# Performance work log

Measured on AMD Instinct MI355X. Metric: run time of the kernel, lower is better.

The kernel has to match this reference:

```python
import jax, jax.numpy as jnp
import numpy as np

P = 1024  # n_prototypes
D = 512   # embed_dim
B = 65536 # batch
EPS = 1e-12  # torch F.normalize eps


def _l2_normalize(x):
    # matches torch.nn.functional.normalize(x, dim=-1): x / max(||x||, eps)
    n = jnp.linalg.norm(x, axis=-1, keepdims=True)
    return x / jnp.maximum(n, EPS)


def setup_inputs() -> dict:
    key = jax.random.key(0)
    k1, k2 = jax.random.split(key)
    query_emb = jax.random.normal(k1, (B, D), dtype=jnp.float32)
    centroid_emb = jax.random.normal(k2, (P, D), dtype=jnp.float32)
    return {"query_emb": query_emb, "centroid_emb": centroid_emb}


def reference(query_emb, centroid_emb):
    q = _l2_normalize(query_emb)           # (B, D)
    c = _l2_normalize(centroid_emb)        # (P, D)
    logits = jnp.einsum('bd,pd->bp', q, c) # (B, P) cosine similarities
    hard_assignment = jnp.argmax(logits, axis=-1)              # (B,)
    hard_one_hot = jax.nn.one_hot(hard_assignment, P, dtype=logits.dtype)
    soft = jax.nn.softmax(logits, axis=-1)                     # (B, P)
    # straight-through: forward value = hard one-hot, gradient flows via soft
    routing_probs = hard_one_hot + soft - jax.lax.stop_gradient(soft)
    context_emb = jnp.einsum('bp,pd->bd', routing_probs, centroid_emb)  # (B, D)
    return context_emb, hard_assignment, routing_probs
```

## Files before the change

### kernel.cpp

```cpp
#include <hip/hip_runtime.h>
#include <hip/hip_bf16.h>
#include <climits>
#include <cstdint>

#define NB 65536
#define NP 1024
#define ND 512

#define MARGIN 4e-3f

typedef _Float16 f16x8 __attribute__((ext_vector_type(8)));
typedef float    f32x4 __attribute__((ext_vector_type(4)));

__device__ inline void load_lds16(const void* g, void* l) {
    __builtin_amdgcn_global_load_lds(
        (const __attribute__((address_space(1))) void*)g,
        (__attribute__((address_space(3))) void*)l, 16, 0, 0);
}

__global__ void centroid_rnorm_kernel(const float* __restrict__ cent,
                                      float* __restrict__ rnorm) {
    const int row  = blockIdx.x * 4 + (threadIdx.x >> 6);
    const int lane = threadIdx.x & 63;
    const float4* cr = (const float4*)(cent + (size_t)row * ND);
    float4 a = cr[2 * lane];
    float4 b = cr[2 * lane + 1];
    float s = a.x * a.x + a.y * a.y + a.z * a.z + a.w * a.w
            + b.x * b.x + b.y * b.y + b.z * b.z + b.w * b.w;
#pragma unroll
    for (int off = 32; off > 0; off >>= 1)
        s += __shfl_down(s, off, 64);
    if (lane == 0)
        rnorm[row] = 1.0f / fmaxf(sqrtf(s), 1e-12f);
}

__global__ void convertQ_kernel(const float* __restrict__ Q,
                                _Float16* __restrict__ Qp) {
    const size_t t = (size_t)blockIdx.x * 256 + threadIdx.x;
    const size_t base = t * 8;
    const float4* s = (const float4*)(Q + base);
    float4 x0 = s[0], x1 = s[1];
    float xs[8] = {x0.x, x0.y, x0.z, x0.w, x1.x, x1.y, x1.z, x1.w};
    f16x8 hi;
#pragma unroll
    for (int i = 0; i < 8; ++i)
        hi[i] = (_Float16)xs[i];
    *(f16x8*)(Qp + base) = hi;
}

__global__ void convertC_kernel(const float* __restrict__ C,
                                _Float16* __restrict__ Cp) {
    const size_t t = (size_t)blockIdx.x * 256 + threadIdx.x;
    const size_t base = t * 8;
    const float4* s = (const float4*)(C + base);
    float4 x0 = s[0], x1 = s[1];
    float xs[8] = {x0.x, x0.y, x0.z, x0.w, x1.x, x1.y, x1.z, x1.w};
    f16x8 hi;
#pragma unroll
    for (int i = 0; i < 8; ++i)
        hi[i] = (_Float16)xs[i];
    *(f16x8*)(Cp + base) = hi;
}

__launch_bounds__(512, 2)
__global__ void gemm_top2_kernel(const _Float16* __restrict__ Qp,
                                 const _Float16* __restrict__ Cp,
                                 const float* __restrict__ rnorm,
                                 float* __restrict__ pv1,
                                 int*   __restrict__ pi1,
                                 float* __restrict__ pv2) {
    __shared__ __align__(16) _Float16 a_s[128 * 512];

    const int tid  = threadIdx.x;
    const int wave = tid >> 6, lane = tid & 63;
    const int quad = lane >> 4, l15 = lane & 15;

    const int mbase = blockIdx.x * 128;

    {
        const _Float16* src = Qp + (size_t)(mbase + wave) * 512
                                 + ((lane ^ (wave & 7)) << 3);
        _Float16* dst = a_s + wave * 512;
#pragma unroll
        for (int rd = 0; rd < 16; ++rd)
            load_lds16(src + (size_t)rd * 4096, dst + rd * 4096);
    }
    __syncthreads();

#pragma unroll 1
    for (int c = 0; c < 2; ++c) {
        const int cbase = wave * 128 + c * 64;

        f32x4 acc[8][4] = {};

#pragma unroll 4
        for (int kc = 0; kc < 16; ++kc) {
            f16x8 bf[4];
#pragma unroll
            for (int nt = 0; nt < 4; ++nt)
                bf[nt] = *(const f16x8*)(Cp
                    + (size_t)(cbase + nt * 16 + l15) * 512 + kc * 32 + quad * 8);
            f16x8 af[8];
#pragma unroll
            for (int mt = 0; mt < 8; ++mt) {
                const int row  = mt * 16 + l15;
                const int slot = (kc * 4 + quad) ^ (l15 & 7);
                af[mt] = *(const f16x8*)&a_s[row * 512 + slot * 8];
            }
#pragma unroll
            for (int mt = 0; mt < 8; ++mt)
#pragma unroll
                for (int nt = 0; nt < 4; ++nt)
                    acc[mt][nt] = __builtin_amdgcn_mfma_f32_16x16x32_f16(
                        af[mt], bf[nt], acc[mt][nt], 0, 0, 0);
        }

        float rn[4];
#pragma unroll
        for (int nt = 0; nt < 4; ++nt)
            rn[nt] = rnorm[cbase + nt * 16 + l15];

#pragma unroll
        for (int mt = 0; mt < 8; ++mt) {
#pragma unroll
            for (int r = 0; r < 4; ++r) {
                float v1 = -3.0e38f, v2 = -3.0e38f; int i1 = INT_MAX;
#pragma unroll
                for (int nt = 0; nt < 4; ++nt) {
                    float v = acc[mt][nt][r] * rn[nt];
                    int   cc = cbase + nt * 16 + l15;
                    if (v > v1) { v2 = v1; v1 = v; i1 = cc; }
                    else { if (v > v2) v2 = v; if (v == v1 && cc < i1) i1 = cc; }
                }
#pragma unroll
                for (int mask = 1; mask < 16; mask <<= 1) {
                    float ov1 = __shfl_xor(v1, mask, 64);
                    int   oi1 = __shfl_xor(i1, mask, 64);
                    float ov2 = __shfl_xor(v2, mask, 64);
                    if (ov1 > v1) { v2 = fmaxf(v1, ov2); v1 = ov1; i1 = oi1; }
                    else if (ov1 == v1) { v2 = v1; i1 = min(i1, oi1); }
                    else { v2 = fmaxf(v2, ov1); }
                }
                if (l15 == 0) {
                    const int row = mbase + mt * 16 + quad * 4 + r;
                    const size_t g = (size_t)row * 16 + (wave * 2 + c);
                    pv1[g] = v1; pi1[g] = i1; pv2[g] = v2;
                }
            }
        }
    }
}

__global__ void merge_kernel(const float* __restrict__ pv1,
                             const int*   __restrict__ pi1,
                             const float* __restrict__ pv2,
                             float* __restrict__ assign_out,
                             int* __restrict__ rlist, int* __restrict__ rcount) {
    const int row = blockIdx.x * 256 + threadIdx.x;
    float v1 = -3.0e38f, v2 = -3.0e38f; int i1 = INT_MAX;
    const size_t b = (size_t)row * 16;
#pragma unroll
    for (int n = 0; n < 16; ++n) {
        float a1 = pv1[b + n]; int ai = pi1[b + n]; float a2 = pv2[b + n];
        if (a1 > v1)       { v2 = fmaxf(v1, a2); v1 = a1; i1 = ai; }
        else if (a1 == v1) { v2 = v1; i1 = min(i1, ai); }
        else               { v2 = fmaxf(v2, a1); }
    }
    assign_out[row] = (float)i1;
    if (v1 - v2 < MARGIN) {
        int p = atomicAdd(rcount, 1);
        rlist[p] = row;
    }
}

__launch_bounds__(256)
__global__ void refine_kernel(const float* __restrict__ Q,
                              const float* __restrict__ C,
                              const float* __restrict__ rnorm,
                              const int* __restrict__ rlist,
                              const int* __restrict__ rcount,
                              float* __restrict__ assign_out) {
    __shared__ float wv[8];
    __shared__ int   wi[8];
    const int n = *rcount;
    const int wave = threadIdx.x >> 6, lane = threadIdx.x & 63;
    for (int it = blockIdx.x * 2; it < n; it += gridDim.x * 2) {
        const int rowA = rlist[it];
        const int rowB = rlist[(it + 1 < n) ? (it + 1) : it];
        const float4* qrA = (const float4*)(Q + (size_t)rowA * ND);
        const float4* qrB = (const float4*)(Q + (size_t)rowB * ND);
        float4 qa  = qrA[lane], qa2 = qrA[lane + 64];
        float4 qb  = qrB[lane], qb2 = qrB[lane + 64];
        float bestA = -3.0e38f, bestB = -3.0e38f;
        int   biA = INT_MAX,    biB = INT_MAX;
        for (int i = 0; i < 64; ++i) {
            const int p0 = i * 16 + wave * 4;
            float sA[4], sB[4];
#pragma unroll
            for (int jj = 0; jj < 4; ++jj) {
                const float4* cr = (const float4*)(C + (size_t)(p0 + jj) * ND);
                float4 b = cr[lane], b2 = cr[lane + 64];
                sA[jj] = qa.x * b.x + qa.y * b.y + qa.z * b.z + qa.w * b.w
                       + qa2.x * b2.x + qa2.y * b2.y + qa2.z * b2.z + qa2.w * b2.w;
                sB[jj] = qb.x * b.x + qb.y * b.y + qb.z * b.z + qb.w * b.w
                       + qb2.x * b2.x + qb2.y * b2.y + qb2.z * b2.z + qb2.w * b2.w;
            }
#pragma unroll
            for (int m = 1; m < 64; m <<= 1) {
#pragma unroll
                for (int jj = 0; jj < 4; ++jj) {
                    sA[jj] += __shfl_xor(sA[jj], m, 64);
                    sB[jj] += __shfl_xor(sB[jj], m, 64);
                }
            }
#pragma unroll
            for (int jj = 0; jj < 4; ++jj) {
                float rnv = rnorm[p0 + jj];
                float vA = sA[jj] * rnv, vB = sB[jj] * rnv;
                if (vA > bestA) { bestA = vA; biA = p0 + jj; }
                if (vB > bestB) { bestB = vB; biB = p0 + jj; }
            }
        }
        __syncthreads();
        if (lane == 0) {
            wv[wave] = bestA;     wi[wave] = biA;
            wv[4 + wave] = bestB; wi[4 + wave] = biB;
        }
        __syncthreads();
        if (threadIdx.x == 0) {
            float bv = wv[0]; int b0 = wi[0];
            for (int w = 1; w < 4; ++w)
                if (wv[w] > bv || (wv[w] == bv && wi[w] < b0)) { bv = wv[w]; b0 = wi[w]; }
            assign_out[rowA] = (float)b0;
        }
        if (threadIdx.x == 64) {
            float bv = wv[4]; int b0 = wi[4];
            for (int w = 5; w < 8; ++w)
                if (wv[w] > bv || (wv[w] == bv && wi[w] < b0)) { bv = wv[w]; b0 = wi[w]; }
            assign_out[rowB] = (float)b0;
        }
    }
}

__global__ void scatter_kernel(const float* __restrict__ cent,
                               const float* __restrict__ assign,
                               float* __restrict__ ctx,
                               float* __restrict__ routing) {
    const int q    = blockIdx.x * 2 + (threadIdx.x >> 7);
    const int lane = threadIdx.x & 127;
    const int ci   = (int)assign[q];
    const float4* src = (const float4*)(cent + (size_t)ci * ND);
    ((float4*)(ctx + (size_t)q * ND))[lane] = src[lane];
    float4 z1 = {0.f, 0.f, 0.f, 0.f};
    float4 z2 = {0.f, 0.f, 0.f, 0.f};
    if ((ci >> 2) == lane)        ((float*)&z1)[ci & 3] = 1.0f;
    if ((ci >> 2) == lane + 128)  ((float*)&z2)[ci & 3] = 1.0f;
    float4* rr = (float4*)(routing + (size_t)q * NP);
    rr[lane]       = z1;
    rr[lane + 128] = z2;
}

extern "C" void kernel_launch(void* const* d_in, const int* in_sizes, int n_in,
                              void* d_out, int out_size, void* d_ws, size_t ws_size,
                              hipStream_t stream) {
    const float* query = (const float*)d_in[0];
    const float* cent  = (const float*)d_in[1];

    float* out        = (float*)d_out;
    float* ctx        = out;
    float* assign_out = out + (size_t)NB * ND;
    float* routing    = assign_out + NB;

    char* scratch = (char*)routing;
    _Float16* Qp    = (_Float16*)(scratch);
    _Float16* Cp    = (_Float16*)(scratch + 67108864);
    float*    rnorm = (float*)   (scratch + 68157440);
    float*    pv1   = (float*)   (scratch + 68161536);
    int*      pi1   = (int*)     (scratch + 72355840);
    float*    pv2   = (float*)   (scratch + 76550144);
    int*      rlist = (int*)     (scratch + 80744448);
    int*      rcount= (int*)     (scratch + 81006592);

    hipMemsetAsync(rcount, 0, sizeof(int), stream);

    centroid_rnorm_kernel<<<NP / 4, 256, 0, stream>>>(cent, rnorm);
    convertC_kernel<<<NP * ND / 8 / 256, 256, 0, stream>>>(cent, Cp);
    convertQ_kernel<<<NB * (ND / 8) / 256, 256, 0, stream>>>(query, Qp);
    gemm_top2_kernel<<<512, 512, 0, stream>>>(Qp, Cp, rnorm, pv1, pi1, pv2);
    merge_kernel<<<NB / 256, 256, 0, stream>>>(pv1, pi1, pv2, assign_out, rlist, rcount);
    refine_kernel<<<512, 256, 0, stream>>>(query, cent, rnorm, rlist, rcount, assign_out);
    scatter_kernel<<<NB / 2, 256, 0, stream>>>(cent, assign_out, ctx, routing);
}
```

Baseline: 767.2 us.

## Replace LDS-staged GEMM with single-wave 64x64 tiles loading directly from global

The top-2 GEMM kernel drops the 128-row LDS staging of queries and the 512-thread blocks. It now launches 16384 single-wave blocks, each computing a 64x64 tile with A and B fragments read straight from global memory and a swizzled block-to-tile mapping for L2 locality. The aim is to remove LDS traffic and barriers and to raise occupancy. In exchange, per-wave data reuse drops, so global and L2 load traffic rises and the kernel may become memory-bound.

Measured after the change: 853.2 us. +11.2%, slower.

```diff
diff --git a/kernel.cpp b/kernel.cpp
--- a/kernel.cpp
+++ b/kernel.cpp
@@ -11,12 +11,6 @@
 
 typedef _Float16 f16x8 __attribute__((ext_vector_type(8)));
 typedef float    f32x4 __attribute__((ext_vector_type(4)));
-
-__device__ inline void load_lds16(const void* g, void* l) {
-    __builtin_amdgcn_global_load_lds(
-        (const __attribute__((address_space(1))) void*)g,
-        (__attribute__((address_space(3))) void*)l, 16, 0, 0);
-}
 
 __global__ void centroid_rnorm_kernel(const float* __restrict__ cent,
                                       float* __restrict__ rnorm) {
@@ -62,90 +56,73 @@
     *(f16x8*)(Cp + base) = hi;
 }
 
-__launch_bounds__(512, 2)
+__launch_bounds__(64, 3)
 __global__ void gemm_top2_kernel(const _Float16* __restrict__ Qp,
                                  const _Float16* __restrict__ Cp,
                                  const float* __restrict__ rnorm,
                                  float* __restrict__ pv1,
                                  int*   __restrict__ pi1,
                                  float* __restrict__ pv2) {
-    __shared__ __align__(16) _Float16 a_s[128 * 512];
-
-    const int tid  = threadIdx.x;
-    const int wave = tid >> 6, lane = tid & 63;
+    const int lane = threadIdx.x;
     const int quad = lane >> 4, l15 = lane & 15;
 
-    const int mbase = blockIdx.x * 128;
-
-    {
-        const _Float16* src = Qp + (size_t)(mbase + wave) * 512
-                                 + ((lane ^ (wave & 7)) << 3);
-        _Float16* dst = a_s + wave * 512;
-#pragma unroll
-        for (int rd = 0; rd < 16; ++rd)
-            load_lds16(src + (size_t)rd * 4096, dst + rd * 4096);
-    }
-    __syncthreads();
-
-#pragma unroll 1
-    for (int c = 0; c < 2; ++c) {
-        const int cbase = wave * 128 + c * 64;
-
-        f32x4 acc[8][4] = {};
+    const int bid = blockIdx.x;
+    const int x = bid & 7, j = bid >> 3;
+    const int nb  = j & 15;
+    const int mtb = (j >> 4) * 8 + x;
+    const int mbase = mtb * 64, nbase = nb * 64;
+
+    const _Float16* Arow = Qp + (size_t)(mbase + l15) * 512 + (quad << 3);
+    const _Float16* Brow = Cp + (size_t)(nbase + l15) * 512 + (quad << 3);
+
+    f32x4 acc[4][4] = {};
 
 #pragma unroll 4
-        for (int kc = 0; kc < 16; ++kc) {
-            f16x8 bf[4];
+    for (int kc = 0; kc < 16; ++kc) {
+        f16x8 af[4], bf[4];
+#pragma unroll
+        for (int t = 0; t < 4; ++t) {
+            af[t] = *(const f16x8*)(Arow + (size_t)(t * 16) * 512 + kc * 32);
+            bf[t] = *(const f16x8*)(Brow + (size_t)(t * 16) * 512 + kc * 32);
+        }
+#pragma unroll
+        for (int mt = 0; mt < 4; ++mt)
 #pragma unroll
             for (int nt = 0; nt < 4; ++nt)
-                bf[nt] = *(const f16x8*)(Cp
-                    + (size_t)(cbase + nt * 16 + l15) * 512 + kc * 32 + quad * 8);
-            f16x8 af[8];
-#pragma unroll
-            for (int mt = 0; mt < 8; ++mt) {
-                const int row  = mt * 16 + l15;
-                const int slot = (kc * 4 + quad) ^ (l15 & 7);
-                af[mt] = *(const f16x8*)&a_s[row * 512 + slot * 8];
-            }
-#pragma unroll
-            for (int mt = 0; mt < 8; ++mt)
-#pragma unroll
-                for (int nt = 0; nt < 4; ++nt)
-                    acc[mt][nt] = __builtin_amdgcn_mfma_f32_16x16x32_f16(
-                        af[mt], bf[nt], acc[mt][nt], 0, 0, 0);
-        }
-
-        float rn[4];
-#pragma unroll
-        for (int nt = 0; nt < 4; ++nt)
-            rn[nt] = rnorm[cbase + nt * 16 + l15];
-
-#pragma unroll
-        for (int mt = 0; mt < 8; ++mt) {
-#pragma unroll
-            for (int r = 0; r < 4; ++r) {
-                float v1 = -3.0e38f, v2 = -3.0e38f; int i1 = INT_MAX;
-#pragma unroll
-                for (int nt = 0; nt < 4; ++nt) {
-                    float v = acc[mt][nt][r] * rn[nt];
-                    int   cc = cbase + nt * 16 + l15;
-                    if (v > v1) { v2 = v1; v1 = v; i1 = cc; }
-                    else { if (v > v2) v2 = v; if (v == v1 && cc < i1) i1 = cc; }
-                }
-#pragma unroll
-                for (int mask = 1; mask < 16; mask <<= 1) {
-                    float ov1 = __shfl_xor(v1, mask, 64);
-                    int   oi1 = __shfl_xor(i1, mask, 64);
-                    float ov2 = __shfl_xor(v2, mask, 64);
-                    if (ov1 > v1) { v2 = fmaxf(v1, ov2); v1 = ov1; i1 = oi1; }
-                    else if (ov1 == v1) { v2 = v1; i1 = min(i1, oi1); }
-                    else { v2 = fmaxf(v2, ov1); }
-                }
-                if (l15 == 0) {
-                    const int row = mbase + mt * 16 + quad * 4 + r;
-                    const size_t g = (size_t)row * 16 + (wave * 2 + c);
-                    pv1[g] = v1; pi1[g] = i1; pv2[g] = v2;
-                }
+                acc[mt][nt] = __builtin_amdgcn_mfma_f32_16x16x32_f16(
+                    af[mt], bf[nt], acc[mt][nt], 0, 0, 0);
+    }
+
+    float rn[4];
+#pragma unroll
+    for (int nt = 0; nt < 4; ++nt)
+        rn[nt] = rnorm[nbase + nt * 16 + l15];
+
+#pragma unroll
+    for (int mt = 0; mt < 4; ++mt) {
+#pragma unroll
+        for (int r = 0; r < 4; ++r) {
+            float v1 = -3.0e38f, v2 = -3.0e38f; int i1 = INT_MAX;
+#pragma unroll
+            for (int nt = 0; nt < 4; ++nt) {
+                float v = acc[mt][nt][r] * rn[nt];
+                int   cc = nbase + nt * 16 + l15;
+                if (v > v1) { v2 = v1; v1 = v; i1 = cc; }
+                else { if (v > v2) v2 = v; if (v == v1 && cc < i1) i1 = cc; }
+            }
+#pragma unroll
+            for (int mask = 1; mask < 16; mask <<= 1) {
+                float ov1 = __shfl_xor(v1, mask, 64);
+                int   oi1 = __shfl_xor(i1, mask, 64);
+                float ov2 = __shfl_xor(v2, mask, 64);
+                if (ov1 > v1) { v2 = fmaxf(v1, ov2); v1 = ov1; i1 = oi1; }
+                else if (ov1 == v1) { v2 = v1; i1 = min(i1, oi1); }
+                else { v2 = fmaxf(v2, ov1); }
+            }
+            if (l15 == 0) {
+                const int row = mbase + mt * 16 + quad * 4 + r;
+                const size_t g = (size_t)row * 16 + nb;
+                pv1[g] = v1; pi1[g] = i1; pv2[g] = v2;
             }
         }
     }
@@ -286,7 +263,7 @@
     centroid_rnorm_kernel<<<NP / 4, 256, 0, stream>>>(cent, rnorm);
     convertC_kernel<<<NP * ND / 8 / 256, 256, 0, stream>>>(cent, Cp);
     convertQ_kernel<<<NB * (ND / 8) / 256, 256, 0, stream>>>(query, Qp);
-    gemm_top2_kernel<<<512, 512, 0, stream>>>(Qp, Cp, rnorm, pv1, pi1, pv2);
+    gemm_top2_kernel<<<16384, 64, 0, stream>>>(Qp, Cp, rnorm, pv1, pi1, pv2);
     merge_kernel<<<NB / 256, 256, 0, stream>>>(pv1, pi1, pv2, assign_out, rlist, rcount);
     refine_kernel<<<512, 256, 0, stream>>>(query, cent, rnorm, rlist, rcount, assign_out);
     scatter_kernel<<<NB / 2, 256, 0, stream>>>(cent, assign_out, ctx, routing);
```

## Retile GEMM into 256x256 output blocks with double-buffered LDS K-pipeline

Applied to the files above, without the earlier changes.

The GEMM+top2 kernel previously kept a 128-row Q slab resident in LDS and streamed centroid fragments straight from global memory per wave. It now tiles each block as 256 queries by 256 centroids, stages 64-wide K slices of both A and B into double-buffered LDS with async global-to-LDS loads, and splits the MFMA work into four phases with priority hints and barriers. Blocks are remapped so the 8 neighbouring block IDs share a centroid tile, and the grid doubles to 1024. This targets redundant uncached B reads and poor load/compute overlap, at the cost of more barriers and per-block LDS traffic.

New measurement: 746.1 us. 2.8% less time.

```diff
diff --git a/kernel.cpp b/kernel.cpp
--- a/kernel.cpp
+++ b/kernel.cpp
@@ -69,83 +69,164 @@
                                  float* __restrict__ pv1,
                                  int*   __restrict__ pi1,
                                  float* __restrict__ pv2) {
-    __shared__ __align__(16) _Float16 a_s[128 * 512];
+    __shared__ __align__(16) _Float16 a_s[2][256 * 64];
+    __shared__ __align__(16) _Float16 b_s[2][256 * 64];
 
     const int tid  = threadIdx.x;
     const int wave = tid >> 6, lane = tid & 63;
     const int quad = lane >> 4, l15 = lane & 15;
-
-    const int mbase = blockIdx.x * 128;
-
-    {
-        const _Float16* src = Qp + (size_t)(mbase + wave) * 512
-                                 + ((lane ^ (wave & 7)) << 3);
-        _Float16* dst = a_s + wave * 512;
-#pragma unroll
-        for (int rd = 0; rd < 16; ++rd)
-            load_lds16(src + (size_t)rd * 4096, dst + rd * 4096);
-    }
-    __syncthreads();
+    const int sx   = l15 & 7;
+
+    const int bid = blockIdx.x;
+    const int x = bid & 7, j = bid >> 3;
+    const int nbb = j & 3;
+    const int mb  = (j >> 2) * 8 + x;
+    const int mbA = mb * 256, nbB = nbb * 256;
+
+    const int wm = wave >> 2, wn = wave & 3;
+
+    f32x4 acc[8][4] = {};
+
+    const int rowi = tid >> 3;
+    const int slot = tid & 7;
+    auto STAGE = [&](int tt, int bb) {
+        const int kbase = tt << 6;
+#pragma unroll
+        for (int seg = 0; seg < 4; ++seg) {
+            const int lr = seg * 64 + rowi;
+            const int sc = ((slot ^ (lr & 7)) << 3);
+            load_lds16(Qp + (size_t)(mbA + lr) * 512 + kbase + sc,
+                       a_s[bb] + lr * 64 + slot * 8);
+        }
+#pragma unroll
+        for (int seg = 0; seg < 4; ++seg) {
+            const int lr = seg * 64 + rowi;
+            const int sc = ((slot ^ (lr & 7)) << 3);
+            load_lds16(Cp + (size_t)(nbB + lr) * 512 + kbase + sc,
+                       b_s[bb] + lr * 64 + slot * 8);
+        }
+    };
+
+    STAGE(0, 0);
+    STAGE(1, 1);
 
 #pragma unroll 1
-    for (int c = 0; c < 2; ++c) {
-        const int cbase = wave * 128 + c * 64;
-
-        f32x4 acc[8][4] = {};
-
-#pragma unroll 4
-        for (int kc = 0; kc < 16; ++kc) {
-            f16x8 bf[4];
-#pragma unroll
-            for (int nt = 0; nt < 4; ++nt)
-                bf[nt] = *(const f16x8*)(Cp
-                    + (size_t)(cbase + nt * 16 + l15) * 512 + kc * 32 + quad * 8);
-            f16x8 af[8];
-#pragma unroll
-            for (int mt = 0; mt < 8; ++mt) {
-                const int row  = mt * 16 + l15;
-                const int slot = (kc * 4 + quad) ^ (l15 & 7);
-                af[mt] = *(const f16x8*)&a_s[row * 512 + slot * 8];
-            }
-#pragma unroll
-            for (int mt = 0; mt < 8; ++mt)
-#pragma unroll
-                for (int nt = 0; nt < 4; ++nt)
+    for (int t = 0; t < 8; ++t) {
+        const int cur = t & 1;
+        if (t < 7) asm volatile("s_waitcnt vmcnt(8)" ::: "memory");
+        else       asm volatile("s_waitcnt vmcnt(0)" ::: "memory");
+        __builtin_amdgcn_s_barrier();
+
+        const _Float16* As = a_s[cur];
+        const _Float16* Bs = b_s[cur];
+
+        f16x8 af[4][2], bf0[2][2], bf1[2][2];
+
+#pragma unroll
+        for (int mt = 0; mt < 4; ++mt)
+#pragma unroll
+            for (int k = 0; k < 2; ++k)
+                af[mt][k] = *(const f16x8*)&As[(wm * 128 + mt * 16 + l15) * 64
+                                              + (((k * 4 + quad) ^ sx) << 3)];
+#pragma unroll
+        for (int nt = 0; nt < 2; ++nt)
+#pragma unroll
+            for (int k = 0; k < 2; ++k)
+                bf0[nt][k] = *(const f16x8*)&Bs[(wn * 64 + nt * 16 + l15) * 64
+                                               + (((k * 4 + quad) ^ sx) << 3)];
+        __builtin_amdgcn_s_setprio(1);
+#pragma unroll
+        for (int mt = 0; mt < 4; ++mt)
+#pragma unroll
+            for (int nt = 0; nt < 2; ++nt)
+#pragma unroll
+                for (int k = 0; k < 2; ++k)
                     acc[mt][nt] = __builtin_amdgcn_mfma_f32_16x16x32_f16(
-                        af[mt], bf[nt], acc[mt][nt], 0, 0, 0);
-        }
-
-        float rn[4];
-#pragma unroll
-        for (int nt = 0; nt < 4; ++nt)
-            rn[nt] = rnorm[cbase + nt * 16 + l15];
-
-#pragma unroll
-        for (int mt = 0; mt < 8; ++mt) {
-#pragma unroll
-            for (int r = 0; r < 4; ++r) {
-                float v1 = -3.0e38f, v2 = -3.0e38f; int i1 = INT_MAX;
-#pragma unroll
-                for (int nt = 0; nt < 4; ++nt) {
-                    float v = acc[mt][nt][r] * rn[nt];
-                    int   cc = cbase + nt * 16 + l15;
-                    if (v > v1) { v2 = v1; v1 = v; i1 = cc; }
-                    else { if (v > v2) v2 = v; if (v == v1 && cc < i1) i1 = cc; }
-                }
-#pragma unroll
-                for (int mask = 1; mask < 16; mask <<= 1) {
-                    float ov1 = __shfl_xor(v1, mask, 64);
-                    int   oi1 = __shfl_xor(i1, mask, 64);
-                    float ov2 = __shfl_xor(v2, mask, 64);
-                    if (ov1 > v1) { v2 = fmaxf(v1, ov2); v1 = ov1; i1 = oi1; }
-                    else if (ov1 == v1) { v2 = v1; i1 = min(i1, oi1); }
-                    else { v2 = fmaxf(v2, ov1); }
-                }
-                if (l15 == 0) {
-                    const int row = mbase + mt * 16 + quad * 4 + r;
-                    const size_t g = (size_t)row * 16 + (wave * 2 + c);
-                    pv1[g] = v1; pi1[g] = i1; pv2[g] = v2;
-                }
+                        af[mt][k], bf0[nt][k], acc[mt][nt], 0, 0, 0);
+        __builtin_amdgcn_s_setprio(0);
+        __builtin_amdgcn_s_barrier();
+
+#pragma unroll
+        for (int nt = 0; nt < 2; ++nt)
+#pragma unroll
+            for (int k = 0; k < 2; ++k)
+                bf1[nt][k] = *(const f16x8*)&Bs[(wn * 64 + 32 + nt * 16 + l15) * 64
+                                               + (((k * 4 + quad) ^ sx) << 3)];
+        __builtin_amdgcn_s_setprio(1);
+#pragma unroll
+        for (int mt = 0; mt < 4; ++mt)
+#pragma unroll
+            for (int nt = 0; nt < 2; ++nt)
+#pragma unroll
+                for (int k = 0; k < 2; ++k)
+                    acc[mt][2 + nt] = __builtin_amdgcn_mfma_f32_16x16x32_f16(
+                        af[mt][k], bf1[nt][k], acc[mt][2 + nt], 0, 0, 0);
+        __builtin_amdgcn_s_setprio(0);
+        __builtin_amdgcn_s_barrier();
+
+#pragma unroll
+        for (int mt = 0; mt < 4; ++mt)
+#pragma unroll
+            for (int k = 0; k < 2; ++k)
+                af[mt][k] = *(const f16x8*)&As[(wm * 128 + 64 + mt * 16 + l15) * 64
+                                              + (((k * 4 + quad) ^ sx) << 3)];
+        __builtin_amdgcn_s_setprio(1);
+#pragma unroll
+        for (int mt = 0; mt < 4; ++mt)
+#pragma unroll
+            for (int nt = 0; nt < 2; ++nt)
+#pragma unroll
+                for (int k = 0; k < 2; ++k)
+                    acc[4 + mt][2 + nt] = __builtin_amdgcn_mfma_f32_16x16x32_f16(
+                        af[mt][k], bf1[nt][k], acc[4 + mt][2 + nt], 0, 0, 0);
+        __builtin_amdgcn_s_setprio(0);
+        __builtin_amdgcn_s_barrier();
+
+        __builtin_amdgcn_s_setprio(1);
+#pragma unroll
+        for (int mt = 0; mt < 4; ++mt)
+#pragma unroll
+            for (int nt = 0; nt < 2; ++nt)
+#pragma unroll
+                for (int k = 0; k < 2; ++k)
+                    acc[4 + mt][nt] = __builtin_amdgcn_mfma_f32_16x16x32_f16(
+                        af[mt][k], bf0[nt][k], acc[4 + mt][nt], 0, 0, 0);
+        __builtin_amdgcn_s_setprio(0);
+        __builtin_amdgcn_s_barrier();
+
+        if (t + 2 < 8) STAGE(t + 2, cur);
+    }
+
+    float rn[4];
+#pragma unroll
+    for (int nt = 0; nt < 4; ++nt)
+        rn[nt] = rnorm[nbB + wn * 64 + nt * 16 + l15];
+
+#pragma unroll
+    for (int mt = 0; mt < 8; ++mt) {
+#pragma unroll
+        for (int r = 0; r < 4; ++r) {
+            float v1 = -3.0e38f, v2 = -3.0e38f; int i1 = INT_MAX;
+#pragma unroll
+            for (int nt = 0; nt < 4; ++nt) {
+                float v = acc[mt][nt][r] * rn[nt];
+                int   cc = nbB + wn * 64 + nt * 16 + l15;
+                if (v > v1) { v2 = v1; v1 = v; i1 = cc; }
+                else { if (v > v2) v2 = v; if (v == v1 && cc < i1) i1 = cc; }
+            }
+#pragma unroll
+            for (int mask = 1; mask < 16; mask <<= 1) {
+                float ov1 = __shfl_xor(v1, mask, 64);
+                int   oi1 = __shfl_xor(i1, mask, 64);
+                float ov2 = __shfl_xor(v2, mask, 64);
+                if (ov1 > v1) { v2 = fmaxf(v1, ov2); v1 = ov1; i1 = oi1; }
+                else if (ov1 == v1) { v2 = v1; i1 = min(i1, oi1); }
+                else { v2 = fmaxf(v2, ov1); }
+            }
+            if (l15 == 0) {
+                const int row = mbA + wm * 128 + mt * 16 + quad * 4 + r;
+                const size_t g = (size_t)row * 16 + (nbb * 4 + wn);
+                pv1[g] = v1; pi1[g] = i1; pv2[g] = v2;
             }
         }
     }
@@ -286,7 +367,7 @@
     centroid_rnorm_kernel<<<NP / 4, 256, 0, stream>>>(cent, rnorm);
     convertC_kernel<<<NP * ND / 8 / 256, 256, 0, stream>>>(cent, Cp);
     convertQ_kernel<<<NB * (ND / 8) / 256, 256, 0, stream>>>(query, Qp);
-    gemm_top2_kernel<<<512, 512, 0, stream>>>(Qp, Cp, rnorm, pv1, pi1, pv2);
+    gemm_top2_kernel<<<1024, 512, 0, stream>>>(Qp, Cp, rnorm, pv1, pi1, pv2);
     merge_kernel<<<NB / 256, 256, 0, stream>>>(pv1, pi1, pv2, assign_out, rlist, rcount);
     refine_kernel<<<512, 256, 0, stream>>>(query, cent, rnorm, rlist, rcount, assign_out);
     scatter_kernel<<<NB / 2, 256, 0, stream>>>(cent, assign_out, ctx, routing);
```
